# Performance work log

Hardware: AMD Instinct MI355X
Metric: run time of the kernel (lower is better)

Reference implementation:

```python
import jax, jax.numpy as jnp
import numpy as np

N, E, ND, ED, HID = 50000, 400000, 128, 64, 128
GIN = 2 * ND + 2  # gnn1 input dim
CIN = 2 * HID + ED  # classifier input dim


def seg_mean(v, idx, n):
    s = jax.ops.segment_sum(v, idx, num_segments=n)
    cnt = jax.ops.segment_sum(jnp.ones((v.shape[0], 1), v.dtype), idx, num_segments=n)
    return s / jnp.maximum(cnt, 1.0)


def layer_norm(h, g, b):
    mu = h.mean(-1, keepdims=True)
    var = ((h - mu) ** 2).mean(-1, keepdims=True)
    return (h - mu) / jnp.sqrt(var + 1e-5) * g + b


def gatv2(h, src, dst, ea, wl, wr, we, att, bias, n, heads):
    # PyG GATv2Conv, concat=False, negative_slope=0.2, add_self_loops with fill_value='mean'
    C = wl.shape[1] // heads
    loop_attr = seg_mean(ea, dst, n)  # self-loop edge_attr = mean of incoming edge_attr
    ar = jnp.arange(n, dtype=src.dtype)
    s = jnp.concatenate([src, ar])
    d = jnp.concatenate([dst, ar])
    ea2 = jnp.concatenate([ea, loop_attr], axis=0)
    xl = (h @ wl).reshape(n, heads, C)
    xr = (h @ wr).reshape(n, heads, C)
    e = xl[s] + xr[d] + (ea2 @ we).reshape(-1, heads, C)  # [E2, H, C]
    e = jax.nn.leaky_relu(e, 0.2)
    logit = (e * att).sum(-1)  # [E2, H]
    m = jax.ops.segment_max(logit, d, num_segments=n)
    m = jnp.where(jnp.isfinite(m), m, 0.0)
    a = jnp.exp(logit - m[d])
    denom = jax.ops.segment_sum(a, d, num_segments=n)
    a = a / jnp.maximum(denom[d], 1e-16)
    out = jax.ops.segment_sum(xl[s] * a[..., None], d, num_segments=n)  # [N, H, C]
    return out.mean(axis=1) + bias


def setup_inputs() -> dict:
    key = jax.random.key(0)
    ks = jax.random.split(key, 32)
    w = lambda k, sh: jax.random.normal(k, sh, jnp.float32) * 0.05
    x = jax.random.normal(ks[0], (N, ND), jnp.float32)
    node_stats = jax.random.uniform(ks[1], (N, 2), jnp.float32)
    src = jax.random.randint(ks[2], (E,), 0, N)
    dst = (src + 1 + jax.random.randint(ks[3], (E,), 0, N - 1)) % N  # guarantees src != dst
    edge_index = jnp.stack([src, dst]).astype(jnp.int32)
    edge_attr = jax.random.normal(ks[4], (E, ED), jnp.float32)
    return {
        'x': x, 'node_stats': node_stats, 'edge_index': edge_index, 'edge_attr': edge_attr,
        'epw': w(ks[5], (ED, ND)), 'epb': jnp.zeros((ND,), jnp.float32),
        'g1wl': w(ks[6], (GIN, 2 * HID)), 'g1wr': w(ks[7], (GIN, 2 * HID)),
        'g1we': w(ks[8], (ED, 2 * HID)), 'g1att': w(ks[9], (2, HID)), 'g1b': jnp.zeros((HID,), jnp.float32),
        'n1g': jnp.ones((HID,), jnp.float32), 'n1b': jnp.zeros((HID,), jnp.float32),
        'g2wl': w(ks[10], (HID, HID)), 'g2wr': w(ks[11], (HID, HID)),
        'g2we': w(ks[12], (ED, HID)), 'g2att': w(ks[13], (1, HID)), 'g2b': jnp.zeros((HID,), jnp.float32),
        'n2g': jnp.ones((HID,), jnp.float32), 'n2b': jnp.zeros((HID,), jnp.float32),
        'c1w': w(ks[14], (CIN, HID)), 'c1b': jnp.zeros((HID,), jnp.float32),
        'c2w': w(ks[15], (HID, HID // 2)), 'c2b': jnp.zeros((HID // 2,), jnp.float32),
        'c3w': w(ks[16], (HID // 2, 1)), 'c3b': jnp.zeros((1,), jnp.float32),
    }


def reference(x, node_stats, edge_index, edge_attr, epw, epb, g1wl, g1wr, g1we, g1att, g1b,
              n1g, n1b, g2wl, g2wr, g2we, g2att, g2b, n2g, n2b, c1w, c1b, c2w, c2b, c3w, c3b):
    src, dst = edge_index[0], edge_index[1]
    n = x.shape[0]
    emb = jax.nn.relu(edge_attr @ epw + epb)  # [E, ND]
    x_out = seg_mean(emb, src, n)
    x_in = seg_mean(emb, dst, n)
    xi = jnp.concatenate([x_out, x_in, node_stats], axis=1)  # [N, GIN]
    h1 = jax.nn.elu(layer_norm(gatv2(xi, src, dst, edge_attr, g1wl, g1wr, g1we, g1att, g1b, n, 2), n1g, n1b))
    h2 = jax.nn.elu(layer_norm(gatv2(h1, src, dst, edge_attr, g2wl, g2wr, g2we, g2att, g2b, n, 1), n2g, n2b))
    er = jnp.concatenate([h2[src], h2[dst], edge_attr], axis=1)  # [E, CIN]
    h = jax.nn.relu(er @ c1w + c1b)
    h = jax.nn.relu(h @ c2w + c2b)
    return h @ c3w + c3b  # [E, 1]
```

## Files before the change

kernel.cpp:

```cpp
#include <hip/hip_runtime.h>
#include <cstdint>
#include <cstddef>


static inline int cdiv(int a, int b) { return (a + b - 1) / b; }

typedef __attribute__((ext_vector_type(8))) short bfrag;
typedef __attribute__((ext_vector_type(4))) float ffrag;

__device__ __forceinline__ float bf2f(unsigned short u) {
  return __uint_as_float(((unsigned)u) << 16);
}
__device__ __forceinline__ unsigned short f2bf(float f) {
  unsigned b = __float_as_uint(f);
  return (unsigned short)((b + 0x7FFFu + ((b >> 16) & 1u)) >> 16);
}

struct PrepJobs {
  const float* src[11];
  unsigned short* dst[11];
  int K[11], Nc[11], KC[11], ld[11];
};
__global__ void prep_bt(PrepJobs J) {
  int j = blockIdx.x;
  int K = J.K[j], Nc = J.Nc[j], KC = J.KC[j], ld = J.ld[j];
  const float* S = J.src[j];
  unsigned short* D = J.dst[j];
  for (int n = blockIdx.y; n < Nc; n += gridDim.y)
    for (int t = threadIdx.x; t < KC; t += blockDim.x) {
      float v = (t < K) ? S[(size_t)t * ld + n] : 0.f;
      D[(size_t)n * KC + t] = f2bf(v);
    }
}

__global__ void count_deg(const int* __restrict__ src, const int* __restrict__ dst,
                          int* __restrict__ dsrc, int* __restrict__ ddst, int E) {
  int t = blockIdx.x * blockDim.x + threadIdx.x;
  if (t < E) {
    atomicAdd(&dsrc[src[t]], 1);
    atomicAdd(&ddst[dst[t]], 1);
  }
}

__global__ __launch_bounds__(256) void scan_local(
    const int* __restrict__ degA, const int* __restrict__ degB,
    int* __restrict__ rowA, int* __restrict__ rowB, int* __restrict__ bsum,
    int N, int nb) {
  __shared__ int s[256];
  int arr = blockIdx.y;
  const int* deg = arr ? degB : degA;
  int* row = arr ? rowB : rowA;
  int b = blockIdx.x;
  int i = b * 256 + threadIdx.x;
  int v = (i < N) ? deg[i] : 0;
  s[threadIdx.x] = v;
  __syncthreads();
  for (int off = 1; off < 256; off <<= 1) {
    int t = (threadIdx.x >= off) ? s[threadIdx.x - off] : 0;
    __syncthreads();
    s[threadIdx.x] += t;
    __syncthreads();
  }
  int incl = s[threadIdx.x];
  if (i < N) row[i] = incl - v;
  if (threadIdx.x == 255) bsum[arr * nb + b] = incl;
}

__global__ __launch_bounds__(1024) void scan_bsums(int* __restrict__ bsum, int nb,
                                                   int* __restrict__ rowA,
                                                   int* __restrict__ rowB, int N) {
  __shared__ int s[1024];
  int tid = threadIdx.x;
  for (int arr = 0; arr < 2; arr++) {
    int v = (tid < nb) ? bsum[arr * nb + tid] : 0;
    s[tid] = v;
    __syncthreads();
    for (int off = 1; off < 1024; off <<= 1) {
      int t = (tid >= off) ? s[tid - off] : 0;
      __syncthreads();
      s[tid] += t;
      __syncthreads();
    }
    if (tid < nb) bsum[arr * nb + tid] = s[tid] - v;
    if (tid == nb - 1) {
      int* row = arr ? rowB : rowA;
      row[N] = s[tid];
    }
    __syncthreads();
  }
}

__global__ void scan_add(int* __restrict__ rowA, int* __restrict__ rowB,
                         int* __restrict__ curA, const int* __restrict__ bsum,
                         int N, int nb) {
  int arr = blockIdx.y;
  int* row = arr ? rowB : rowA;
  int b = blockIdx.x;
  int i = b * 256 + threadIdx.x;
  if (i < N) {
    int v = row[i] + bsum[arr * nb + b];
    row[i] = v;
    if (arr == 0) curA[i] = v;
  }
}

__global__ void ext_fix(const int* __restrict__ row_dst, int* __restrict__ row_ext,
                        int* __restrict__ cur_ext, int* __restrict__ ext_eid,
                        int E, int N) {
  int i = blockIdx.x * blockDim.x + threadIdx.x;
  if (i <= N) row_ext[i] = row_dst[i] + i;
  if (i < N) {
    cur_ext[i] = row_dst[i] + i;
    ext_eid[row_dst[i + 1] + i] = E + i;
  }
}

__global__ void scatter_eid(const int* __restrict__ src, const int* __restrict__ dst,
                            int* __restrict__ csrc, int* __restrict__ cext,
                            int* __restrict__ esrc, int* __restrict__ ext_eid,
                            int E) {
  int t = blockIdx.x * blockDim.x + threadIdx.x;
  if (t < E) {
    int p = atomicAdd(&csrc[src[t]], 1);
    esrc[p] = t;
    int q = atomicAdd(&cext[dst[t]], 1);
    ext_eid[q] = t;
  }
}

struct ASrc {
  const float *p0, *p1, *p2;
  int ld0, ld1, ld2, k0, k1;
};
__device__ __forceinline__ float loadA(const ASrc& a, int m, int k) {
  if (k < a.k0) return a.p0[(size_t)m * a.ld0 + k];
  if (k < a.k1) return a.p1[(size_t)m * a.ld1 + (k - a.k0)];
  return a.p2[(size_t)m * a.ld2 + (k - a.k1)];
}
__device__ __forceinline__ int regionOf(const ASrc& a, int k) {
  return k < a.k0 ? 0 : (k < a.k1 ? 1 : 2);
}

template <int ACT, int OBF, int ABF>
__global__ __launch_bounds__(256) void gemm_mfma(
    ASrc A, const unsigned short* __restrict__ Abf, int lda,
    const unsigned short* __restrict__ Bt, int ldbt,
    const float* __restrict__ bias, void* __restrict__ Cv, int ldc, int M, int K) {
  __shared__ __align__(16) unsigned short asb[64 * 72];
  __shared__ __align__(16) unsigned short bsb[128 * 72];
  int tid = threadIdx.x;
  int m0 = blockIdx.x * 64, n0 = blockIdx.y * 128;
  int lane = tid & 63, wave = tid >> 6;
  int quad = lane >> 4, l16 = lane & 15;
  ffrag zero = {0.f, 0.f, 0.f, 0.f};
  ffrag acc[8];
#pragma unroll
  for (int t = 0; t < 8; t++) acc[t] = zero;
  int KC = (K + 63) & ~63;
  for (int kc = 0; kc < KC; kc += 64) {
    __syncthreads();
    {
      int row = tid & 63, kq = tid >> 6;
      int gm = m0 + row;
      if (ABF) {
        const unsigned short* rp = Abf + (size_t)gm * lda + kc + kq * 16;
        ushort4 z = make_ushort4(0, 0, 0, 0);
#pragma unroll
        for (int q = 0; q < 4; q++) {
          ushort4 v = (gm < M) ? *(const ushort4*)(rp + q * 4) : z;
          *(ushort4*)&asb[row * 72 + kq * 16 + q * 4] = v;
        }
      } else {
        bool fastc = (kc + 64 <= K) && (regionOf(A, kc) == regionOf(A, kc + 63)) &&
                     (gm < M);
        if (fastc) {
          int r = regionOf(A, kc);
          const float* p;
          int ld, koff;
          if (r == 0) { p = A.p0; ld = A.ld0; koff = 0; }
          else if (r == 1) { p = A.p1; ld = A.ld1; koff = A.k0; }
          else { p = A.p2; ld = A.ld2; koff = A.k1; }
          const float* rp = p + (size_t)gm * ld + (kc - koff) + kq * 16;
#pragma unroll
          for (int q = 0; q < 4; q++) {
            float4 v = *(const float4*)(rp + q * 4);
            *(ushort4*)&asb[row * 72 + kq * 16 + q * 4] =
                make_ushort4(f2bf(v.x), f2bf(v.y), f2bf(v.z), f2bf(v.w));
          }
        } else {
#pragma unroll
          for (int q = 0; q < 16; q++) {
            int kk = kc + kq * 16 + q;
            float v = (gm < M && kk < K) ? loadA(A, gm, kk) : 0.f;
            asb[row * 72 + kq * 16 + q] = f2bf(v);
          }
        }
      }
    }
    {
      int n = tid >> 1, hf = tid & 1;
      const ushort4* rp = (const ushort4*)(Bt + (size_t)(n0 + n) * ldbt + kc + hf * 32);
      ushort4* dp = (ushort4*)&bsb[n * 72 + hf * 32];
#pragma unroll
      for (int i = 0; i < 8; i++) dp[i] = rp[i];
    }
    __syncthreads();
    int arow = wave * 16 + l16;
    bfrag a0 = *(const bfrag*)&asb[arow * 72 + quad * 8];
    bfrag a1 = *(const bfrag*)&asb[arow * 72 + 32 + quad * 8];
#pragma unroll
    for (int t = 0; t < 8; t++) {
      int bn = t * 16 + l16;
      bfrag b0 = *(const bfrag*)&bsb[bn * 72 + quad * 8];
      bfrag b1 = *(const bfrag*)&bsb[bn * 72 + 32 + quad * 8];
      acc[t] = __builtin_amdgcn_mfma_f32_16x16x32_bf16(a0, b0, acc[t], 0, 0, 0);
      acc[t] = __builtin_amdgcn_mfma_f32_16x16x32_bf16(a1, b1, acc[t], 0, 0, 0);
    }
  }
#pragma unroll
  for (int t = 0; t < 8; t++) {
    int col = n0 + t * 16 + l16;
    float bv = bias ? bias[col] : 0.f;
#pragma unroll
    for (int r = 0; r < 4; r++) {
      int row = m0 + wave * 16 + quad * 4 + r;
      if (row < M) {
        float v = acc[t][r] + bv;
        if (ACT == 1) v = fmaxf(v, 0.f);
        if (OBF)
          ((unsigned short*)Cv)[(size_t)row * ldc + col] = f2bf(v);
        else
          ((float*)Cv)[(size_t)row * ldc + col] = v;
      }
    }
  }
}

__global__ __launch_bounds__(256) void gather_mean(
    const int* __restrict__ row_src, const int* __restrict__ eid_src,
    const int* __restrict__ row_ext, const int* __restrict__ ext_eid,
    const unsigned short* __restrict__ emb, const float* __restrict__ ea,
    float* __restrict__ xout, float* __restrict__ xin, float* __restrict__ lattr,
    int N) {
  int lane = threadIdx.x & 63, wid = threadIdx.x >> 6;
  int n = blockIdx.x * 4 + wid;
  int side = blockIdx.y;
  if (n >= N) return;
  int lo, hi;
  const int* eid;
  if (side) { lo = row_ext[n]; hi = row_ext[n + 1] - 1; eid = ext_eid; }
  else { lo = row_src[n]; hi = row_src[n + 1]; eid = eid_src; }
  float a0 = 0.f, a1 = 0.f, la = 0.f;
  for (int j = lo; j < hi; j++) {
    int e = eid[j];
    ushort2 v = *(const ushort2*)&emb[(size_t)e * 128 + lane * 2];
    a0 += bf2f(v.x);
    a1 += bf2f(v.y);
    if (side) la += ea[(size_t)e * 64 + lane];
  }
  float r = 1.f / fmaxf((float)(hi - lo), 1.f);
  float* ob = side ? xin : xout;
  *(float2*)&ob[(size_t)n * 128 + lane * 2] = make_float2(a0 * r, a1 * r);
  if (side) lattr[(size_t)n * 64 + lane] = la * r;
}

template <int H>
__global__ __launch_bounds__(256) void attn_logits_mfma(
    const unsigned short* __restrict__ xl, const unsigned short* __restrict__ xr,
    const int* __restrict__ src, const int* __restrict__ dst,
    const float* __restrict__ ea, const float* __restrict__ lattr,
    const unsigned short* __restrict__ wet, const float* __restrict__ att,
    float* __restrict__ lg, int E, int N) {
  constexpr int HC = H * 128;
  __shared__ __align__(16) unsigned short asb[64 * 72];
  __shared__ __align__(16) unsigned short bsb[128 * 72];
  __shared__ float atts[128];
  __shared__ int sidx[64], didx[64];
  unsigned short* Cs = bsb;
  int tid = threadIdx.x;
  int E2 = E + N;
  int i0 = blockIdx.x * 64;
  int lane = tid & 63, wave = tid >> 6, quad = lane >> 4, l16 = lane & 15;
  if (tid < 64) {
    int gi = i0 + tid;
    int s = 0, d = 0;
    if (gi < E2) {
      if (gi < E) { s = src[gi]; d = dst[gi]; }
      else { s = d = gi - E; }
    }
    sidx[tid] = s;
    didx[tid] = d;
  }
  {
    int row = tid & 63, kq = tid >> 6;
    int gi = i0 + row;
    if (gi < E2) {
      const float* ap =
          (gi < E) ? ea + (size_t)gi * 64 : lattr + (size_t)(gi - E) * 64;
      const float* rp = ap + kq * 16;
#pragma unroll
      for (int q = 0; q < 4; q++) {
        float4 v = *(const float4*)(rp + q * 4);
        *(ushort4*)&asb[row * 72 + kq * 16 + q * 4] =
            make_ushort4(f2bf(v.x), f2bf(v.y), f2bf(v.z), f2bf(v.w));
      }
    } else {
      ushort4 z = make_ushort4(0, 0, 0, 0);
#pragma unroll
      for (int q = 0; q < 4; q++) *(ushort4*)&asb[row * 72 + kq * 16 + q * 4] = z;
    }
  }
  int er = tid >> 4, cc = tid & 15;
  ffrag zero = {0.f, 0.f, 0.f, 0.f};
  for (int head = 0; head < H; head++) {
    int n0 = head * 128;
    __syncthreads();
    if (tid < 128) atts[tid] = att[n0 + tid];
    {
      int n = tid >> 1, hf = tid & 1;
      const ushort4* rp = (const ushort4*)(wet + (size_t)(n0 + n) * 64 + hf * 32);
      ushort4* dp = (ushort4*)&bsb[n * 72 + hf * 32];
#pragma unroll
      for (int i = 0; i < 8; i++) dp[i] = rp[i];
    }
    __syncthreads();
    int arow = wave * 16 + l16;
    bfrag a0 = *(const bfrag*)&asb[arow * 72 + quad * 8];
    bfrag a1 = *(const bfrag*)&asb[arow * 72 + 32 + quad * 8];
    ffrag acc[8];
#pragma unroll
    for (int t = 0; t < 8; t++) {
      acc[t] = zero;
      int bn = t * 16 + l16;
      bfrag b0 = *(const bfrag*)&bsb[bn * 72 + quad * 8];
      bfrag b1 = *(const bfrag*)&bsb[bn * 72 + 32 + quad * 8];
      acc[t] = __builtin_amdgcn_mfma_f32_16x16x32_bf16(a0, b0, acc[t], 0, 0, 0);
      acc[t] = __builtin_amdgcn_mfma_f32_16x16x32_bf16(a1, b1, acc[t], 0, 0, 0);
    }
    __syncthreads();
    {
      int rb = wave * 16 + quad * 4;
#pragma unroll
      for (int t = 0; t < 8; t++)
#pragma unroll
        for (int r = 0; r < 4; r++)
          Cs[(rb + r) * 136 + t * 16 + l16] = f2bf(acc[t][r]);
    }
    __syncthreads();
#pragma unroll
    for (int i2 = 0; i2 < 4; i2++) {
      int r = er * 4 + i2;
      int gi = i0 + r;
      float ps = 0.f;
      if (gi < E2) {
        int s = sidx[r], d = didx[r];
#pragma unroll
        for (int h = 0; h < 2; h++) {
          int c = h * 64 + cc * 4;
          ushort4 mv = *(const ushort4*)&Cs[r * 136 + c];
          ushort4 xlu = *(const ushort4*)&xl[(size_t)s * HC + n0 + c];
          ushort4 xru = *(const ushort4*)&xr[(size_t)d * HC + n0 + c];
          float e0 = bf2f(mv.x) + bf2f(xlu.x) + bf2f(xru.x);
          float e1 = bf2f(mv.y) + bf2f(xlu.y) + bf2f(xru.y);
          float e2 = bf2f(mv.z) + bf2f(xlu.z) + bf2f(xru.z);
          float e3 = bf2f(mv.w) + bf2f(xlu.w) + bf2f(xru.w);
          e0 = e0 > 0.f ? e0 : 0.2f * e0;
          e1 = e1 > 0.f ? e1 : 0.2f * e1;
          e2 = e2 > 0.f ? e2 : 0.2f * e2;
          e3 = e3 > 0.f ? e3 : 0.2f * e3;
          ps += e0 * atts[c + 0] + e1 * atts[c + 1] + e2 * atts[c + 2] +
                e3 * atts[c + 3];
        }
      }
      ps += __shfl_xor(ps, 1);
      ps += __shfl_xor(ps, 2);
      ps += __shfl_xor(ps, 4);
      ps += __shfl_xor(ps, 8);
      if (cc == 0 && gi < E2) lg[(size_t)gi * H + head] = ps;
    }
  }
}

template <int H>
__global__ __launch_bounds__(256) void attn_fused(
    const unsigned short* __restrict__ xl, const float* __restrict__ lg,
    const int* __restrict__ row_ext, const int* __restrict__ ext_eid,
    const int* __restrict__ src, const float* __restrict__ bias,
    const float* __restrict__ gam, const float* __restrict__ bet,
    unsigned short* __restrict__ hout, int E, int N) {
  constexpr int HC = H * 128;
  constexpr int CPL = HC / 64;
  int lane = threadIdx.x & 63, wid = threadIdx.x >> 6;
  int n = blockIdx.x * 4 + wid;
  if (n >= N) return;
  int lo = row_ext[n], hi = row_ext[n + 1];
  int myh = (H == 2) ? (lane >> 5) : 0;
  int colbase = (H == 2) ? (myh * 128 + (lane & 31) * 4) : (lane * 2);
  float m = -3.4e38f;
  for (int j = lo; j < hi; j++) m = fmaxf(m, lg[(size_t)ext_eid[j] * H + myh]);
  float asum = 0.f;
  float acc[CPL] = {};
  for (int j = lo; j < hi; j++) {
    int e = ext_eid[j];
    int s = (e < E) ? src[e] : (e - E);
    float a = __expf(lg[(size_t)e * H + myh] - m);
    asum += a;
    const unsigned short* xp = &xl[(size_t)s * HC + colbase];
    if (H == 2) {
      ushort4 u = *(const ushort4*)xp;
      acc[0] += a * bf2f(u.x);
      acc[1] += a * bf2f(u.y);
      acc[2] += a * bf2f(u.z);
      acc[3] += a * bf2f(u.w);
    } else {
      ushort2 u = *(const ushort2*)xp;
      acc[0] += a * bf2f(u.x);
      acc[1] += a * bf2f(u.y);
    }
  }
  float inv = 1.f / fmaxf(asum, 1e-16f);
#pragma unroll
  for (int k = 0; k < CPL; k++) acc[k] *= inv;
  int ch;
  if (H == 2) {
#pragma unroll
    for (int k = 0; k < CPL; k++) acc[k] = (acc[k] + __shfl_xor(acc[k], 32)) * 0.5f;
    ch = (lane & 31) * CPL;
  } else {
    ch = lane * CPL;
  }
#pragma unroll
  for (int k = 0; k < CPL; k++) acc[k] += bias[ch + k];
  float s = 0.f;
#pragma unroll
  for (int k = 0; k < CPL; k++) s += acc[k];
#pragma unroll
  for (int mm = 1; mm < 64; mm <<= 1) s += __shfl_xor(s, mm);
  constexpr float dupn = (H == 2) ? 256.f : 128.f;
  float mu = s / dupn;
  float vs = 0.f;
#pragma unroll
  for (int k = 0; k < CPL; k++) {
    acc[k] -= mu;
    vs += acc[k] * acc[k];
  }
#pragma unroll
  for (int mm = 1; mm < 64; mm <<= 1) vs += __shfl_xor(vs, mm);
  float rstd = rsqrtf(vs / dupn + 1e-5f);
  float y[CPL];
#pragma unroll
  for (int k = 0; k < CPL; k++) {
    float v = acc[k] * rstd * gam[ch + k] + bet[ch + k];
    y[k] = v > 0.f ? v : expm1f(v);
  }
  if (H == 2) {
    if (lane < 32)
      *(ushort4*)&hout[(size_t)n * 128 + ch] =
          make_ushort4(f2bf(y[0]), f2bf(y[1]), f2bf(y[2]), f2bf(y[3]));
  } else {
    *(ushort2*)&hout[(size_t)n * 128 + ch] = make_ushort2(f2bf(y[0]), f2bf(y[1]));
  }
}

__global__ __launch_bounds__(256) void classifier_mfma(
    const float* __restrict__ ea, const unsigned short* __restrict__ Wct,
    const int* __restrict__ src, const int* __restrict__ dst,
    const float* __restrict__ P, const float* __restrict__ Q,
    const float* __restrict__ c1b, const unsigned short* __restrict__ c2t,
    const float* __restrict__ c2b, const float* __restrict__ c3w,
    const float* __restrict__ c3b, float* __restrict__ out, int E) {
  __shared__ __align__(16) unsigned short asb[64 * 72];
  __shared__ __align__(16) unsigned short bsb[128 * 72];
  __shared__ __align__(16) unsigned short t1s[64 * 136];
  __shared__ float c1bs[128];
  __shared__ float c2bs[64], c3ws[64];
  __shared__ int sidx[64], didx[64];
  int tid = threadIdx.x;
  int e0 = blockIdx.x * 64;
  int lane = tid & 63, wave = tid >> 6, quad = lane >> 4, l16 = lane & 15;
  if (tid < 128) c1bs[tid] = c1b[tid];
  if (tid < 64) {
    c2bs[tid] = c2b[tid];
    c3ws[tid] = c3w[tid];
    int gi = e0 + tid;
    sidx[tid] = gi < E ? src[gi] : 0;
    didx[tid] = gi < E ? dst[gi] : 0;
  }
  {
    int row = tid & 63, kq = tid >> 6;
    int gi = e0 + row;
    if (gi < E) {
      const float* rp = ea + (size_t)gi * 64 + kq * 16;
#pragma unroll
      for (int q = 0; q < 4; q++) {
        float4 v = *(const float4*)(rp + q * 4);
        *(ushort4*)&asb[row * 72 + kq * 16 + q * 4] =
            make_ushort4(f2bf(v.x), f2bf(v.y), f2bf(v.z), f2bf(v.w));
      }
    } else {
      ushort4 z = make_ushort4(0, 0, 0, 0);
#pragma unroll
      for (int q = 0; q < 4; q++) *(ushort4*)&asb[row * 72 + kq * 16 + q * 4] = z;
    }
  }
  {
    int n = tid >> 1, hf = tid & 1;
    const ushort4* rp = (const ushort4*)(Wct + (size_t)n * 64 + hf * 32);
    ushort4* dp = (ushort4*)&bsb[n * 72 + hf * 32];
#pragma unroll
    for (int i = 0; i < 8; i++) dp[i] = rp[i];
  }
  __syncthreads();
  ffrag zero = {0.f, 0.f, 0.f, 0.f};
  int arow = wave * 16 + l16;
  {
    bfrag a0 = *(const bfrag*)&asb[arow * 72 + quad * 8];
    bfrag a1 = *(const bfrag*)&asb[arow * 72 + 32 + quad * 8];
    ffrag acc[8];
#pragma unroll
    for (int t = 0; t < 8; t++) {
      acc[t] = zero;
      int bn = t * 16 + l16;
      bfrag b0 = *(const bfrag*)&bsb[bn * 72 + quad * 8];
      bfrag b1 = *(const bfrag*)&bsb[bn * 72 + 32 + quad * 8];
      acc[t] = __builtin_amdgcn_mfma_f32_16x16x32_bf16(a0, b0, acc[t], 0, 0, 0);
      acc[t] = __builtin_amdgcn_mfma_f32_16x16x32_bf16(a1, b1, acc[t], 0, 0, 0);
    }
    __syncthreads();
    int rb = wave * 16 + quad * 4;
#pragma unroll
    for (int t = 0; t < 8; t++)
#pragma unroll
      for (int r = 0; r < 4; r++)
        t1s[(rb + r) * 136 + t * 16 + l16] = f2bf(acc[t][r]);
  }
  __syncthreads();
  {
    int erow = tid >> 4, ccc = tid & 15;
#pragma unroll
    for (int i2 = 0; i2 < 4; i2++) {
      int r = erow * 4 + i2;
      int s = sidx[r], d = didx[r];
#pragma unroll
      for (int h = 0; h < 2; h++) {
        int c = h * 64 + ccc * 4;
        ushort4 mv = *(const ushort4*)&t1s[r * 136 + c];
        float4 pv = *(const float4*)&P[(size_t)s * 128 + c];
        float4 qv = *(const float4*)&Q[(size_t)d * 128 + c];
        float v0 = fmaxf(bf2f(mv.x) + pv.x + qv.x + c1bs[c + 0], 0.f);
        float v1 = fmaxf(bf2f(mv.y) + pv.y + qv.y + c1bs[c + 1], 0.f);
        float v2 = fmaxf(bf2f(mv.z) + pv.z + qv.z + c1bs[c + 2], 0.f);
        float v3 = fmaxf(bf2f(mv.w) + pv.w + qv.w + c1bs[c + 3], 0.f);
        *(ushort4*)&t1s[r * 136 + c] =
            make_ushort4(f2bf(v0), f2bf(v1), f2bf(v2), f2bf(v3));
      }
    }
    int n = tid >> 2, qq = tid & 3;
    const ushort4* rp = (const ushort4*)(c2t + (size_t)n * 128 + qq * 32);
    ushort4* dp = (ushort4*)&bsb[n * 136 + qq * 32];
#pragma unroll
    for (int i = 0; i < 8; i++) dp[i] = rp[i];
  }
  __syncthreads();
  {
    bfrag pa[4];
#pragma unroll
    for (int kc = 0; kc < 4; kc++)
      pa[kc] = *(const bfrag*)&t1s[arow * 136 + kc * 32 + quad * 8];
    ffrag acc2[4];
#pragma unroll
    for (int t = 0; t < 4; t++) {
      acc2[t] = zero;
      int bn = t * 16 + l16;
#pragma unroll
      for (int kc = 0; kc < 4; kc++) {
        bfrag b = *(const bfrag*)&bsb[bn * 136 + kc * 32 + quad * 8];
        acc2[t] = __builtin_amdgcn_mfma_f32_16x16x32_bf16(pa[kc], b, acc2[t], 0, 0, 0);
      }
    }
    float c3b0 = c3b[0];
    float rsum[4] = {0.f, 0.f, 0.f, 0.f};
#pragma unroll
    for (int t = 0; t < 4; t++) {
      int col = t * 16 + l16;
      float cb = c2bs[col], cw = c3ws[col];
#pragma unroll
      for (int r = 0; r < 4; r++)
        rsum[r] += fmaxf(acc2[t][r] + cb, 0.f) * cw;
    }
#pragma unroll
    for (int r = 0; r < 4; r++) {
      rsum[r] += __shfl_xor(rsum[r], 1);
      rsum[r] += __shfl_xor(rsum[r], 2);
      rsum[r] += __shfl_xor(rsum[r], 4);
      rsum[r] += __shfl_xor(rsum[r], 8);
    }
    if (l16 == 0) {
#pragma unroll
      for (int r = 0; r < 4; r++) {
        int gi = e0 + wave * 16 + quad * 4 + r;
        if (gi < E) out[gi] = rsum[r] + c3b0;
      }
    }
  }
}

extern "C" void kernel_launch(void* const* d_in, const int* in_sizes, int n_in,
                              void* d_out, int out_size, void* d_ws, size_t ws_size,
                              hipStream_t stream) {
  const int N = in_sizes[1] / 2;
  const int E = in_sizes[3] / 64;
  const int E2 = E + N;
  const int nb = cdiv(N, 256);

  const float* node_stats = (const float*)d_in[1];
  const int* src = (const int*)d_in[2];
  const int* dst = (const int*)d_in[2] + E;
  const float* edge_attr = (const float*)d_in[3];
  const float* epw = (const float*)d_in[4];
  const float* epb = (const float*)d_in[5];
  const float* g1wl = (const float*)d_in[6];
  const float* g1wr = (const float*)d_in[7];
  const float* g1we = (const float*)d_in[8];
  const float* g1att = (const float*)d_in[9];
  const float* g1b = (const float*)d_in[10];
  const float* n1g = (const float*)d_in[11];
  const float* n1b = (const float*)d_in[12];
  const float* g2wl = (const float*)d_in[13];
  const float* g2wr = (const float*)d_in[14];
  const float* g2we = (const float*)d_in[15];
  const float* g2att = (const float*)d_in[16];
  const float* g2b = (const float*)d_in[17];
  const float* n2g = (const float*)d_in[18];
  const float* n2b = (const float*)d_in[19];
  const float* c1w = (const float*)d_in[20];
  const float* c1b = (const float*)d_in[21];
  const float* c2w = (const float*)d_in[22];
  const float* c2b = (const float*)d_in[23];
  const float* c3w = (const float*)d_in[24];
  const float* c3b = (const float*)d_in[25];
  float* out = (float*)d_out;

  float* w = (float*)d_ws;
  size_t o = 0;
  auto alloc = [&](size_t n) { float* p = w + o; o += n; return p; };
  float* xout = alloc((size_t)N * 128);
  float* xin = alloc((size_t)N * 128);
  float* lattr = alloc((size_t)N * 64);
  float* lg = alloc((size_t)E2 * 2);
  int* row_src = (int*)alloc((size_t)(N + 1));
  int* row_dst = (int*)alloc((size_t)(N + 1));
  int* row_ext = (int*)alloc((size_t)(N + 1));
  int* deg_src = (int*)alloc((size_t)N);
  int* deg_dst = (int*)alloc((size_t)N);
  int* cur_src = (int*)alloc((size_t)N);
  int* cur_ext = (int*)alloc((size_t)N);
  int* eid_src = (int*)alloc((size_t)E);
  int* ext_eid = (int*)alloc((size_t)E2);
  int* bsum = (int*)alloc((size_t)2 * 1024);
  unsigned short* wb = (unsigned short*)alloc(140000);
  float* R = alloc((size_t)E * 64);
  unsigned short* Ru = (unsigned short*)R;
  unsigned short* emb = Ru;
  unsigned short* xl1b = Ru;
  unsigned short* xr1b = Ru + (size_t)N * 256;
  unsigned short* h1b = Ru + (size_t)N * 512;
  unsigned short* xl2b = Ru + (size_t)N * 640;
  unsigned short* xr2b = Ru + (size_t)N * 768;
  unsigned short* h2b = Ru + (size_t)N * 896;
  float* P = xout;
  float* Q = xin;

  unsigned short* epwt = wb + 0;
  unsigned short* g1wlt = wb + 8192;
  unsigned short* g1wrt = wb + 90112;
  unsigned short* g1wet = wb + 172032;
  unsigned short* g2wlt = wb + 188416;
  unsigned short* g2wrt = wb + 204800;
  unsigned short* g2wet = wb + 221184;
  unsigned short* c1wat = wb + 229376;
  unsigned short* c1wbt = wb + 245760;
  unsigned short* c1wct = wb + 262144;
  unsigned short* c2t = wb + 270336;

  PrepJobs J;
  auto setj = [&](int i, const float* s, unsigned short* d2, int K, int Nc,
                  int KC, int ld) {
    J.src[i] = s; J.dst[i] = d2; J.K[i] = K; J.Nc[i] = Nc; J.KC[i] = KC; J.ld[i] = ld;
  };
  setj(0, epw, epwt, 64, 128, 64, 128);
  setj(1, g1wl, g1wlt, 258, 256, 320, 256);
  setj(2, g1wr, g1wrt, 258, 256, 320, 256);
  setj(3, g1we, g1wet, 64, 256, 64, 256);
  setj(4, g2wl, g2wlt, 128, 128, 128, 128);
  setj(5, g2wr, g2wrt, 128, 128, 128, 128);
  setj(6, g2we, g2wet, 64, 128, 64, 128);
  setj(7, c1w, c1wat, 128, 128, 128, 128);
  setj(8, c1w + 128 * 128, c1wbt, 128, 128, 128, 128);
  setj(9, c1w + 256 * 128, c1wct, 64, 128, 64, 128);
  setj(10, c2w, c2t, 128, 64, 128, 64);
  prep_bt<<<dim3(11, 32), 256, 0, stream>>>(J);

  hipMemsetAsync(deg_src, 0, (size_t)2 * N * sizeof(int), stream);
  count_deg<<<cdiv(E, 256), 256, 0, stream>>>(src, dst, deg_src, deg_dst, E);
  scan_local<<<dim3(nb, 2), 256, 0, stream>>>(deg_src, deg_dst, row_src, row_dst,
                                              bsum, N, nb);
  scan_bsums<<<1, 1024, 0, stream>>>(bsum, nb, row_src, row_dst, N);
  scan_add<<<dim3(nb, 2), 256, 0, stream>>>(row_src, row_dst, cur_src, bsum, N, nb);
  ext_fix<<<cdiv(N + 1, 256), 256, 0, stream>>>(row_dst, row_ext, cur_ext,
                                                ext_eid, E, N);
  scatter_eid<<<cdiv(E, 256), 256, 0, stream>>>(src, dst, cur_src, cur_ext,
                                                eid_src, ext_eid, E);

  ASrc dummy{nullptr, nullptr, nullptr, 0, 0, 0, 0, 0};

  {
    ASrc a{edge_attr, nullptr, nullptr, 64, 0, 0, 64, 64};
    gemm_mfma<1, 1, 0><<<dim3(cdiv(E, 64), 1), 256, 0, stream>>>(
        a, nullptr, 0, epwt, 64, epb, emb, 128, E, 64);
  }
  gather_mean<<<dim3(cdiv(N, 4), 2), 256, 0, stream>>>(
      row_src, eid_src, row_ext, ext_eid, emb, edge_attr, xout, xin, lattr, N);

  {
    ASrc a{xout, xin, node_stats, 128, 128, 2, 128, 256};
    dim3 g(cdiv(N, 64), 2);
    gemm_mfma<0, 1, 0><<<g, 256, 0, stream>>>(a, nullptr, 0, g1wlt, 320, nullptr,
                                              xl1b, 256, N, 258);
    gemm_mfma<0, 1, 0><<<g, 256, 0, stream>>>(a, nullptr, 0, g1wrt, 320, nullptr,
                                              xr1b, 256, N, 258);
  }

  attn_logits_mfma<2><<<cdiv(E2, 64), 256, 0, stream>>>(
      xl1b, xr1b, src, dst, edge_attr, lattr, g1wet, g1att, lg, E, N);
  attn_fused<2><<<cdiv(N, 4), 256, 0, stream>>>(xl1b, lg, row_ext, ext_eid, src,
                                                g1b, n1g, n1b, h1b, E, N);

  {
    dim3 g(cdiv(N, 64), 1);
    gemm_mfma<0, 1, 1><<<g, 256, 0, stream>>>(dummy, h1b, 128, g2wlt, 128,
                                              nullptr, xl2b, 128, N, 128);
    gemm_mfma<0, 1, 1><<<g, 256, 0, stream>>>(dummy, h1b, 128, g2wrt, 128,
                                              nullptr, xr2b, 128, N, 128);
  }

  attn_logits_mfma<1><<<cdiv(E2, 64), 256, 0, stream>>>(
      xl2b, xr2b, src, dst, edge_attr, lattr, g2wet, g2att, lg, E, N);
  attn_fused<1><<<cdiv(N, 4), 256, 0, stream>>>(xl2b, lg, row_ext, ext_eid, src,
                                                g2b, n2g, n2b, h2b, E, N);

  {
    dim3 g(cdiv(N, 64), 1);
    gemm_mfma<0, 0, 1><<<g, 256, 0, stream>>>(dummy, h2b, 128, c1wat, 128,
                                              nullptr, P, 128, N, 128);
    gemm_mfma<0, 0, 1><<<g, 256, 0, stream>>>(dummy, h2b, 128, c1wbt, 128,
                                              nullptr, Q, 128, N, 128);
  }
  classifier_mfma<<<cdiv(E, 64), 256, 0, stream>>>(
      edge_attr, c1wct, src, dst, P, Q, c1b, c2t, c2b, c3w, c3b, out, E);
}
```

Baseline: 1.068 ms.

## Pre-convert edge_attr to bf16 and process edges in CSR-sorted order

```diff
diff --git a/kernel.cpp b/kernel.cpp
--- a/kernel.cpp
+++ b/kernel.cpp
@@ -31,6 +31,16 @@
       float v = (t < K) ? S[(size_t)t * ld + n] : 0.f;
       D[(size_t)n * KC + t] = f2bf(v);
     }
+}
+
+__global__ __launch_bounds__(256) void cvt_bf16(const float* __restrict__ in,
+                                                unsigned short* __restrict__ out,
+                                                int n4) {
+  for (int i = blockIdx.x * blockDim.x + threadIdx.x; i < n4;
+       i += gridDim.x * blockDim.x) {
+    float4 v = ((const float4*)in)[i];
+    ((ushort4*)out)[i] = make_ushort4(f2bf(v.x), f2bf(v.y), f2bf(v.z), f2bf(v.w));
+  }
 }
 
 __global__ void count_deg(const int* __restrict__ src, const int* __restrict__ dst,
@@ -239,9 +249,9 @@
 __global__ __launch_bounds__(256) void gather_mean(
     const int* __restrict__ row_src, const int* __restrict__ eid_src,
     const int* __restrict__ row_ext, const int* __restrict__ ext_eid,
-    const unsigned short* __restrict__ emb, const float* __restrict__ ea,
-    float* __restrict__ xout, float* __restrict__ xin, float* __restrict__ lattr,
-    int N) {
+    const unsigned short* __restrict__ emb, const unsigned short* __restrict__ eab,
+    float* __restrict__ xout, float* __restrict__ xin,
+    unsigned short* __restrict__ lattrb, int N) {
   int lane = threadIdx.x & 63, wid = threadIdx.x >> 6;
   int n = blockIdx.x * 4 + wid;
   int side = blockIdx.y;
@@ -256,19 +266,20 @@
     ushort2 v = *(const ushort2*)&emb[(size_t)e * 128 + lane * 2];
     a0 += bf2f(v.x);
     a1 += bf2f(v.y);
-    if (side) la += ea[(size_t)e * 64 + lane];
+    if (side) la += bf2f(eab[(size_t)e * 64 + lane]);
   }
   float r = 1.f / fmaxf((float)(hi - lo), 1.f);
   float* ob = side ? xin : xout;
   *(float2*)&ob[(size_t)n * 128 + lane * 2] = make_float2(a0 * r, a1 * r);
-  if (side) lattr[(size_t)n * 64 + lane] = la * r;
+  if (side) lattrb[(size_t)n * 64 + lane] = f2bf(la * r);
 }
 
 template <int H>
 __global__ __launch_bounds__(256) void attn_logits_mfma(
     const unsigned short* __restrict__ xl, const unsigned short* __restrict__ xr,
     const int* __restrict__ src, const int* __restrict__ dst,
-    const float* __restrict__ ea, const float* __restrict__ lattr,
+    const unsigned short* __restrict__ eab, const unsigned short* __restrict__ lattrb,
+    const int* __restrict__ ext_eid,
     const unsigned short* __restrict__ wet, const float* __restrict__ att,
     float* __restrict__ lg, int E, int N) {
   constexpr int HC = H * 128;
@@ -282,28 +293,27 @@
   int i0 = blockIdx.x * 64;
   int lane = tid & 63, wave = tid >> 6, quad = lane >> 4, l16 = lane & 15;
   if (tid < 64) {
-    int gi = i0 + tid;
+    int j = i0 + tid;
     int s = 0, d = 0;
-    if (gi < E2) {
-      if (gi < E) { s = src[gi]; d = dst[gi]; }
-      else { s = d = gi - E; }
+    if (j < E2) {
+      int e = ext_eid[j];
+      if (e < E) { s = src[e]; d = dst[e]; }
+      else { s = d = e - E; }
     }
     sidx[tid] = s;
     didx[tid] = d;
   }
   {
     int row = tid & 63, kq = tid >> 6;
-    int gi = i0 + row;
-    if (gi < E2) {
-      const float* ap =
-          (gi < E) ? ea + (size_t)gi * 64 : lattr + (size_t)(gi - E) * 64;
-      const float* rp = ap + kq * 16;
-#pragma unroll
-      for (int q = 0; q < 4; q++) {
-        float4 v = *(const float4*)(rp + q * 4);
-        *(ushort4*)&asb[row * 72 + kq * 16 + q * 4] =
-            make_ushort4(f2bf(v.x), f2bf(v.y), f2bf(v.z), f2bf(v.w));
-      }
+    int j = i0 + row;
+    if (j < E2) {
+      int e = ext_eid[j];
+      const unsigned short* ap =
+          (e < E) ? eab + (size_t)e * 64 : lattrb + (size_t)(e - E) * 64;
+      const ushort4* rp = (const ushort4*)(ap + kq * 16);
+#pragma unroll
+      for (int q = 0; q < 4; q++)
+        *(ushort4*)&asb[row * 72 + kq * 16 + q * 4] = rp[q];
     } else {
       ushort4 z = make_ushort4(0, 0, 0, 0);
 #pragma unroll
@@ -397,13 +407,13 @@
   int myh = (H == 2) ? (lane >> 5) : 0;
   int colbase = (H == 2) ? (myh * 128 + (lane & 31) * 4) : (lane * 2);
   float m = -3.4e38f;
-  for (int j = lo; j < hi; j++) m = fmaxf(m, lg[(size_t)ext_eid[j] * H + myh]);
+  for (int j = lo; j < hi; j++) m = fmaxf(m, lg[(size_t)j * H + myh]);
   float asum = 0.f;
   float acc[CPL] = {};
   for (int j = lo; j < hi; j++) {
     int e = ext_eid[j];
     int s = (e < E) ? src[e] : (e - E);
-    float a = __expf(lg[(size_t)e * H + myh] - m);
+    float a = __expf(lg[(size_t)j * H + myh] - m);
     asum += a;
     const unsigned short* xp = &xl[(size_t)s * HC + colbase];
     if (H == 2) {
@@ -463,7 +473,8 @@
 }
 
 __global__ __launch_bounds__(256) void classifier_mfma(
-    const float* __restrict__ ea, const unsigned short* __restrict__ Wct,
+    const unsigned short* __restrict__ eab, const unsigned short* __restrict__ Wct,
+    const int* __restrict__ eid_src,
     const int* __restrict__ src, const int* __restrict__ dst,
     const float* __restrict__ P, const float* __restrict__ Q,
     const float* __restrict__ c1b, const unsigned short* __restrict__ c2t,
@@ -474,7 +485,7 @@
   __shared__ __align__(16) unsigned short t1s[64 * 136];
   __shared__ float c1bs[128];
   __shared__ float c2bs[64], c3ws[64];
-  __shared__ int sidx[64], didx[64];
+  __shared__ int sidx[64], didx[64], eidx[64];
   int tid = threadIdx.x;
   int e0 = blockIdx.x * 64;
   int lane = tid & 63, wave = tid >> 6, quad = lane >> 4, l16 = lane & 15;
@@ -482,21 +493,21 @@
   if (tid < 64) {
     c2bs[tid] = c2b[tid];
     c3ws[tid] = c3w[tid];
-    int gi = e0 + tid;
-    sidx[tid] = gi < E ? src[gi] : 0;
-    didx[tid] = gi < E ? dst[gi] : 0;
+    int j = e0 + tid;
+    int e = (j < E) ? eid_src[j] : 0;
+    eidx[tid] = (j < E) ? e : -1;
+    sidx[tid] = src[e];
+    didx[tid] = dst[e];
   }
   {
     int row = tid & 63, kq = tid >> 6;
-    int gi = e0 + row;
-    if (gi < E) {
-      const float* rp = ea + (size_t)gi * 64 + kq * 16;
-#pragma unroll
-      for (int q = 0; q < 4; q++) {
-        float4 v = *(const float4*)(rp + q * 4);
-        *(ushort4*)&asb[row * 72 + kq * 16 + q * 4] =
-            make_ushort4(f2bf(v.x), f2bf(v.y), f2bf(v.z), f2bf(v.w));
-      }
+    int j = e0 + row;
+    if (j < E) {
+      int e = eid_src[j];
+      const ushort4* rp = (const ushort4*)(eab + (size_t)e * 64 + kq * 16);
+#pragma unroll
+      for (int q = 0; q < 4; q++)
+        *(ushort4*)&asb[row * 72 + kq * 16 + q * 4] = rp[q];
     } else {
       ushort4 z = make_ushort4(0, 0, 0, 0);
 #pragma unroll
@@ -598,8 +609,8 @@
     if (l16 == 0) {
 #pragma unroll
       for (int r = 0; r < 4; r++) {
-        int gi = e0 + wave * 16 + quad * 4 + r;
-        if (gi < E) out[gi] = rsum[r] + c3b0;
+        int e = eidx[wave * 16 + quad * 4 + r];
+        if (e >= 0) out[e] = rsum[r] + c3b0;
       }
     }
   }
@@ -659,6 +670,7 @@
   int* ext_eid = (int*)alloc((size_t)E2);
   int* bsum = (int*)alloc((size_t)2 * 1024);
   unsigned short* wb = (unsigned short*)alloc(140000);
+  unsigned short* eab = (unsigned short*)alloc((size_t)E * 32);
   float* R = alloc((size_t)E * 64);
   unsigned short* Ru = (unsigned short*)R;
   unsigned short* emb = Ru;
@@ -668,6 +680,7 @@
   unsigned short* xl2b = Ru + (size_t)N * 640;
   unsigned short* xr2b = Ru + (size_t)N * 768;
   unsigned short* h2b = Ru + (size_t)N * 896;
+  unsigned short* lattrb = (unsigned short*)lattr;
   float* P = xout;
   float* Q = xin;
 
@@ -683,6 +696,7 @@
   unsigned short* c1wct = wb + 262144;
   unsigned short* c2t = wb + 270336;
 
+  cvt_bf16<<<2048, 256, 0, stream>>>(edge_attr, eab, E * 16);
   PrepJobs J;
   auto setj = [&](int i, const float* s, unsigned short* d2, int K, int Nc,
                   int KC, int ld) {
@@ -714,13 +728,10 @@
 
   ASrc dummy{nullptr, nullptr, nullptr, 0, 0, 0, 0, 0};
 
-  {
-    ASrc a{edge_attr, nullptr, nullptr, 64, 0, 0, 64, 64};
-    gemm_mfma<1, 1, 0><<<dim3(cdiv(E, 64), 1), 256, 0, stream>>>(
-        a, nullptr, 0, epwt, 64, epb, emb, 128, E, 64);
-  }
+  gemm_mfma<1, 1, 1><<<dim3(cdiv(E, 64), 1), 256, 0, stream>>>(
+      dummy, eab, 64, epwt, 64, epb, emb, 128, E, 64);
   gather_mean<<<dim3(cdiv(N, 4), 2), 256, 0, stream>>>(
-      row_src, eid_src, row_ext, ext_eid, emb, edge_attr, xout, xin, lattr, N);
+      row_src, eid_src, row_ext, ext_eid, emb, eab, xout, xin, lattrb, N);
 
   {
     ASrc a{xout, xin, node_stats, 128, 128, 2, 128, 256};
@@ -732,7 +743,7 @@
   }
 
   attn_logits_mfma<2><<<cdiv(E2, 64), 256, 0, stream>>>(
-      xl1b, xr1b, src, dst, edge_attr, lattr, g1wet, g1att, lg, E, N);
+      xl1b, xr1b, src, dst, eab, lattrb, ext_eid, g1wet, g1att, lg, E, N);
   attn_fused<2><<<cdiv(N, 4), 256, 0, stream>>>(xl1b, lg, row_ext, ext_eid, src,
                                                 g1b, n1g, n1b, h1b, E, N);
 
@@ -745,7 +756,7 @@
   }
 
   attn_logits_mfma<1><<<cdiv(E2, 64), 256, 0, stream>>>(
-      xl2b, xr2b, src, dst, edge_attr, lattr, g2wet, g2att, lg, E, N);
+      xl2b, xr2b, src, dst, eab, lattrb, ext_eid, g2wet, g2att, lg, E, N);
   attn_fused<1><<<cdiv(N, 4), 256, 0, stream>>>(xl2b, lg, row_ext, ext_eid, src,
                                                 g2b, n2g, n2b, h2b, E, N);
 
@@ -757,5 +768,5 @@
                                               nullptr, Q, 128, N, 128);
   }
   classifier_mfma<<<cdiv(E, 64), 256, 0, stream>>>(
-      edge_attr, c1wct, src, dst, P, Q, c1b, c2t, c2b, c3w, c3b, out, E);
-}
+      eab, c1wct, eid_src, src, dst, P, Q, c1b, c2t, c2b, c3w, c3b, out, E);
+}
```

Result: faster. 1.035 ms (-3.0%).
